# Optimization experiments

Measured on AMD Instinct MI355X. Metric: run time of the kernel, lower is better.

The kernel has to match this reference:

```python
import jax, jax.numpy as jnp
import numpy as np

N_NODES = 100000
N_EDGES = 1600000
IN_FEATS = 128
H1 = 256
H2 = 256
N_CLASSES = 64


def setup_inputs() -> dict:
    key = jax.random.key(0)
    ks = jax.random.split(key, 12)
    x = jax.random.normal(ks[0], (N_NODES, IN_FEATS), dtype=jnp.float32)
    src = jax.random.randint(ks[1], (N_EDGES,), 0, N_NODES, dtype=jnp.int64 if jax.config.jax_enable_x64 else jnp.int32)
    dst = jax.random.randint(ks[2], (N_EDGES,), 0, N_NODES, dtype=jnp.int64 if jax.config.jax_enable_x64 else jnp.int32)
    def lin(kw, kb, fan_in, fan_out):
        bound = 1.0 / np.sqrt(fan_in)
        W = jax.random.uniform(kw, (fan_out, fan_in), minval=-bound, maxval=bound, dtype=jnp.float32)
        b = jax.random.uniform(kb, (fan_out,), minval=-bound, maxval=bound, dtype=jnp.float32)
        return W, b
    W1, b1 = lin(ks[3], ks[4], 2 * IN_FEATS, H1)
    W2, b2 = lin(ks[5], ks[6], 2 * H1, H2)
    W3, b3 = lin(ks[7], ks[8], 2 * H2, N_CLASSES)
    return {"x": x, "src": src, "dst": dst,
            "W1": W1, "b1": b1, "W2": W2, "b2": b2, "W3": W3, "b3": b3}


def _sage_conv(h, src, dst, W, b):
    # message = copy from src node, reduce = mean at dst node (DGL copy_u + mean)
    m = jnp.take(h, src, axis=0)                                  # [E, d]
    s = jax.ops.segment_sum(m, dst, num_segments=N_NODES)         # [N, d]
    deg = jax.ops.segment_sum(jnp.ones((m.shape[0],), h.dtype), dst,
                              num_segments=N_NODES)               # [N]
    h_N = s / jnp.maximum(deg, 1.0)[:, None]                      # isolated nodes -> 0 (DGL behavior)
    h_total = jnp.concatenate([h, h_N], axis=1)                   # [N, 2d]
    return h_total @ W.T + b                                      # dropout inactive at eval (p=0.05)


def reference(x, src, dst, W1, b1, W2, b2, W3, b3):
    h = jax.nn.relu(_sage_conv(x, src, dst, W1, b1))
    h = jax.nn.relu(_sage_conv(h, src, dst, W2, b2))
    return _sage_conv(h, src, dst, W3, b3)
```

## Files before the change

kernel.cpp:

```cpp
#include <hip/hip_runtime.h>
#include <hip/hip_bf16.h>
#include <cstdint>
#include <cstddef>

#define N_NODES 100000
#define N_EDGES 1600000
#define NBUCK   128
#define NPB     782
#define NB_E    ((N_EDGES + 4095) / 4096)

#define FK_X    NB_E
#define FK_W1   (FK_X + 12500)
#define FK_W2   (FK_W1 + 64)
#define FK_W3   (FK_W2 + 128)
#define FK_END  (FK_W3 + 32)

typedef __attribute__((ext_vector_type(8))) short short8;
typedef __attribute__((ext_vector_type(4))) float floatx4;

__device__ inline float bf_lo(unsigned int u) { return __uint_as_float(u << 16); }
__device__ inline float bf_hi(unsigned int u) { return __uint_as_float(u & 0xffff0000u); }
__device__ inline unsigned short f2bf(float f) {
  unsigned int u = __float_as_uint(f);
  u += 0x7fffu + ((u >> 16) & 1u);
  return (unsigned short)(u >> 16);
}

__device__ inline void cvt4_body(const float* __restrict__ in,
                                 unsigned short* __restrict__ out, int t) {
  float4 v = ((const float4*)in)[t];
  ushort4 o;
  o.x = f2bf(v.x); o.y = f2bf(v.y); o.z = f2bf(v.z); o.w = f2bf(v.w);
  ((ushort4*)out)[t] = o;
}

__global__ __launch_bounds__(256)
void front_kernel(const int* __restrict__ dst, int* __restrict__ blockHist,
                  const float* __restrict__ x,  unsigned short* __restrict__ H0,
                  const float* __restrict__ W1, unsigned short* __restrict__ Wb1,
                  const float* __restrict__ W2, unsigned short* __restrict__ Wb2,
                  const float* __restrict__ W3, unsigned short* __restrict__ Wb3) {
  __shared__ int hist[NBUCK];
  const int b = blockIdx.x, tid = threadIdx.x;
  if (b < FK_X) {
    if (tid < NBUCK) hist[tid] = 0;
    __syncthreads();
#pragma unroll
    for (int i = 0; i < 16; ++i) {
      int e = b * 4096 + i * 256 + tid;
      if (e < N_EDGES) atomicAdd(&hist[dst[e] / NPB], 1);
    }
    __syncthreads();
    if (tid < NBUCK) blockHist[b * NBUCK + tid] = hist[tid];
  } else if (b < FK_W1) {
    cvt4_body(x, H0, (b - FK_X) * 256 + tid);
  } else if (b < FK_W2) {
    cvt4_body(W1, Wb1, (b - FK_W1) * 256 + tid);
  } else if (b < FK_W3) {
    cvt4_body(W2, Wb2, (b - FK_W2) * 256 + tid);
  } else {
    int t = (b - FK_W3) * 256 + tid;
    int idx4 = t * 4;
    int r = idx4 >> 8, c = idx4 & 255;
    float4 v = *(const float4*)(W3 + (size_t)(r & 63) * 512 + (r >> 6) * 256 + c);
    ushort4 o;
    o.x = f2bf(v.x); o.y = f2bf(v.y); o.z = f2bf(v.z); o.w = f2bf(v.w);
    *(ushort4*)(Wb3 + (size_t)r * 256 + c) = o;
  }
}

__device__ inline int wave_incl_scan(int v, int lane) {
#pragma unroll
  for (int off = 1; off < 64; off <<= 1) {
    int t = __shfl_up(v, off, 64);
    if (lane >= off) v += t;
  }
  return v;
}

__global__ void scanB_kernel(const int* __restrict__ blockHist,
                             int* __restrict__ bucketBase, int* __restrict__ blockOfs) {
  __shared__ int wsum[2];
  int t = threadIdx.x, lane = t & 63, wid = t >> 6;
  int total = 0;
#pragma unroll 4
  for (int blk = 0; blk < NB_E; ++blk) total += blockHist[blk * NBUCK + t];
  int incl = wave_incl_scan(total, lane);
  if (lane == 63) wsum[wid] = incl;
  __syncthreads();
  int off = (wid == 1) ? wsum[0] : 0;
  int base = off + incl - total;
  bucketBase[t] = base;
  if (t == 127) bucketBase[NBUCK] = off + incl;
  int running = base;
#pragma unroll 4
  for (int blk = 0; blk < NB_E; ++blk) {
    blockOfs[blk * NBUCK + t] = running;
    running += blockHist[blk * NBUCK + t];
  }
}

__global__ __launch_bounds__(256)
void pass1b_kernel(const int* __restrict__ src, const int* __restrict__ dst,
                   const int* __restrict__ blockOfs, unsigned int* __restrict__ staging) {
  __shared__ int hist[NBUCK];
  if (threadIdx.x < NBUCK) hist[threadIdx.x] = blockOfs[blockIdx.x * NBUCK + threadIdx.x];
  __syncthreads();
#pragma unroll
  for (int i = 0; i < 16; ++i) {
    int e = blockIdx.x * 4096 + i * 256 + threadIdx.x;
    if (e < N_EDGES) {
      int d = dst[e];
      int b = d / NPB;
      int pos = atomicAdd(&hist[b], 1);
      staging[pos] = (unsigned)src[e] | ((unsigned)(d - b * NPB) << 17);
    }
  }
}

__global__ __launch_bounds__(1024)
void pass2_kernel(const unsigned int* __restrict__ staging, const int* __restrict__ bucketBase,
                  int* __restrict__ start, float* __restrict__ invdeg,
                  int* __restrict__ esrc) {
  __shared__ int cnt[1024];
  __shared__ int cur[1024];
  __shared__ int wsum[16];
  const int b = blockIdx.x, tid = threadIdx.x;
  const int lane = tid & 63, wid = tid >> 6;
  const int n0 = b * NPB, n1 = min(n0 + NPB, N_NODES);
  const int nLocal = n1 - n0;
  const int p0 = bucketBase[b], p1 = bucketBase[b + 1];

  cnt[tid] = 0;
  __syncthreads();
  for (int e = p0 + tid; e < p1; e += 1024)
    atomicAdd(&cnt[staging[e] >> 17], 1);
  __syncthreads();

  int c = cnt[tid];
  int incl = wave_incl_scan(c, lane);
  if (lane == 63) wsum[wid] = incl;
  __syncthreads();
  if (wid == 0) {
    int v = (lane < 16) ? wsum[lane] : 0;
    int i2 = wave_incl_scan(v, lane);
    if (lane < 16) wsum[lane] = i2 - v;
  }
  __syncthreads();
  int excl = wsum[wid] + incl - c;
  cur[tid] = excl;
  if (tid < nLocal) {
    start[n0 + tid] = p0 + excl;
    invdeg[n0 + tid] = 1.0f / fmaxf((float)c, 1.0f);
  }
  if (b == NBUCK - 1 && tid == 0) start[N_NODES] = N_EDGES;
  __syncthreads();

  for (int e = p0 + tid; e < p1; e += 1024) {
    unsigned int pr = staging[e];
    int pos = p0 + atomicAdd(&cur[pr >> 17], 1);
    esrc[pos] = (int)(pr & 0x1FFFFu);
  }
}

template<int D>
__global__ __launch_bounds__(256)
void gather_mean(const unsigned short* __restrict__ h,
                 const int* __restrict__ start,
                 const int* __restrict__ esrc,
                 const float* __restrict__ invdeg,
                 unsigned short* __restrict__ hn) {
  int wave = (int)((blockIdx.x * 256 + threadIdx.x) >> 6);
  if (wave >= N_NODES) return;
  int lane = threadIdx.x & 63;
  int s0 = start[wave], s1 = start[wave + 1];
  constexpr int FPL = D / 64;
  float acc[FPL] = {};
  const unsigned short* base = h + lane * FPL;

  int e = s0;
  if constexpr (FPL == 4) {
    for (; e + 4 <= s1; e += 4) {
      int sn0 = esrc[e], sn1 = esrc[e + 1], sn2 = esrc[e + 2], sn3 = esrc[e + 3];
      uint2 p0 = *(const uint2*)(base + (size_t)sn0 * D);
      uint2 p1 = *(const uint2*)(base + (size_t)sn1 * D);
      uint2 p2 = *(const uint2*)(base + (size_t)sn2 * D);
      uint2 p3 = *(const uint2*)(base + (size_t)sn3 * D);
      acc[0] += bf_lo(p0.x) + bf_lo(p1.x) + bf_lo(p2.x) + bf_lo(p3.x);
      acc[1] += bf_hi(p0.x) + bf_hi(p1.x) + bf_hi(p2.x) + bf_hi(p3.x);
      acc[2] += bf_lo(p0.y) + bf_lo(p1.y) + bf_lo(p2.y) + bf_lo(p3.y);
      acc[3] += bf_hi(p0.y) + bf_hi(p1.y) + bf_hi(p2.y) + bf_hi(p3.y);
    }
    for (; e < s1; ++e) {
      int sn = esrc[e];
      uint2 p = *(const uint2*)(base + (size_t)sn * D);
      acc[0] += bf_lo(p.x); acc[1] += bf_hi(p.x);
      acc[2] += bf_lo(p.y); acc[3] += bf_hi(p.y);
    }
  } else {
    for (; e + 4 <= s1; e += 4) {
      int sn0 = esrc[e], sn1 = esrc[e + 1], sn2 = esrc[e + 2], sn3 = esrc[e + 3];
      unsigned int p0 = *(const unsigned int*)(base + (size_t)sn0 * D);
      unsigned int p1 = *(const unsigned int*)(base + (size_t)sn1 * D);
      unsigned int p2 = *(const unsigned int*)(base + (size_t)sn2 * D);
      unsigned int p3 = *(const unsigned int*)(base + (size_t)sn3 * D);
      acc[0] += bf_lo(p0) + bf_lo(p1) + bf_lo(p2) + bf_lo(p3);
      acc[1] += bf_hi(p0) + bf_hi(p1) + bf_hi(p2) + bf_hi(p3);
    }
    for (; e < s1; ++e) {
      int sn = esrc[e];
      unsigned int p = *(const unsigned int*)(base + (size_t)sn * D);
      acc[0] += bf_lo(p); acc[1] += bf_hi(p);
    }
  }

  float inv = invdeg[wave];
  unsigned short* out = hn + (size_t)wave * D + lane * FPL;
  if constexpr (FPL == 4) {
    ushort4 o;
    o.x = f2bf(acc[0] * inv); o.y = f2bf(acc[1] * inv);
    o.z = f2bf(acc[2] * inv); o.w = f2bf(acc[3] * inv);
    *(ushort4*)out = o;
  } else {
    ushort2 o;
    o.x = f2bf(acc[0] * inv); o.y = f2bf(acc[1] * inv);
    *(ushort2*)out = o;
  }
}

__global__ __launch_bounds__(256)
void gather_add64(const unsigned short* __restrict__ Y3,
                  const int* __restrict__ start, const int* __restrict__ esrc,
                  const float* __restrict__ invdeg, float* __restrict__ out) {
  int wave = (int)((blockIdx.x * 256 + threadIdx.x) >> 6);
  if (wave >= N_NODES) return;
  int lane = threadIdx.x & 63;
  int half = lane >> 5, l32 = lane & 31;
  int s0 = start[wave], s1 = start[wave + 1];
  const unsigned short* ybase = Y3 + 2 * l32;
  float a0 = 0.f, a1 = 0.f, b0 = 0.f, b1 = 0.f;
  for (int base = s0 + half; base < s1; base += 16) {
    unsigned int p[8];
#pragma unroll
    for (int k = 0; k < 8; ++k) {
      int e = base + 2 * k;
      p[k] = (e < s1) ? *(const unsigned int*)(ybase + (size_t)esrc[e] * 64) : 0u;
    }
#pragma unroll
    for (int k = 0; k < 8; k += 2) {
      a0 += bf_lo(p[k]);     a1 += bf_hi(p[k]);
      b0 += bf_lo(p[k + 1]); b1 += bf_hi(p[k + 1]);
    }
  }
  a0 += b0; a1 += b1;
  a0 += __shfl_xor(a0, 32, 64);
  a1 += __shfl_xor(a1, 32, 64);
  if (half == 0) {
    float inv = invdeg[wave];
    float2* q = (float2*)(out + (size_t)wave * 64 + 2 * l32);
    float2 v = *q;
    v.x += inv * a0; v.y += inv * a1;
    *q = v;
  }
}

template<int D, int DOUT, int BN, bool RELU, bool OUTF32, int MODE>
__global__ __launch_bounds__(256)
void sage_gemm(const unsigned short* __restrict__ H,
               const unsigned short* __restrict__ HN,
               const unsigned short* __restrict__ Wb,
               const float* __restrict__ bias,
               void* __restrict__ outp,
               unsigned short* __restrict__ y3) {
  constexpr int K   = (MODE == 1) ? D : 2 * D;
  constexpr int BM  = 128, KC = 32;
  constexpr int NCHUNK = K / KC;
  constexpr int AF  = BM / 16;
  constexpr int BF  = BN / 16;
  constexpr int FR  = AF + BF;
  constexpr int NMF = 4;
  constexpr int NJF = BF / 2;

  __shared__ __align__(16) unsigned short lds0[FR * 512];
  __shared__ __align__(16) unsigned short lds1[FR * 512];

  const int tid  = threadIdx.x;
  const int wave = tid >> 6, lane = tid & 63;
  const int l16  = lane & 15, quad = lane >> 4;
  const int n0   = blockIdx.x * BM;
  const int bn0  = blockIdx.y * BN;
  const int wm   = wave >> 1, wn = wave & 1;

  floatx4 acc[NMF][NJF] = {};

  auto stage = [&](int c, unsigned short* buf) {
    const int kc = c * KC;
    const unsigned short* srcH = (kc < D) ? H : HN;
    const int kb = (kc < D) ? kc : kc - D;
    const int w0 = __builtin_amdgcn_readfirstlane(wave);
#pragma unroll
    for (int i = 0; i < FR / 4; ++i) {
      const int fu = w0 + 4 * i;
      const unsigned short* g;
      if (fu < AF) {
        int row = min(n0 + fu * 16 + l16, N_NODES - 1);
        g = srcH + (size_t)row * D + kb + quad * 8;
      } else {
        int col = bn0 + (fu - AF) * 16 + l16;
        g = Wb + (size_t)col * K + kc + quad * 8;
      }
      __builtin_amdgcn_global_load_lds(
          (const __attribute__((address_space(1))) unsigned int*)g,
          (__attribute__((address_space(3))) unsigned int*)(buf + fu * 512),
          16, 0, 0);
    }
  };

  auto compute = [&](const unsigned short* buf) {
    short8 b[NJF];
#pragma unroll
    for (int jt = 0; jt < NJF; ++jt)
      b[jt] = *(const short8*)(buf + (AF + wn * NJF + jt) * 512 + lane * 8);
#pragma unroll
    for (int mi = 0; mi < NMF; ++mi) {
      short8 a = *(const short8*)(buf + (wm * NMF + mi) * 512 + lane * 8);
#pragma unroll
      for (int jt = 0; jt < NJF; ++jt)
        acc[mi][jt] = __builtin_amdgcn_mfma_f32_16x16x32_bf16(a, b[jt], acc[mi][jt], 0, 0, 0);
    }
  };

  stage(0, lds0);
  __syncthreads();
#pragma unroll 1
  for (int c = 0; c < NCHUNK; c += 2) {
    stage(c + 1, lds1);
    compute(lds0);
    __syncthreads();
    if (c + 2 < NCHUNK) stage(c + 2, lds0);
    compute(lds1);
    __syncthreads();
  }

#pragma unroll
  for (int mi = 0; mi < NMF; ++mi) {
#pragma unroll
    for (int jt = 0; jt < NJF; ++jt) {
      int j = bn0 + wn * (NJF * 16) + jt * 16 + l16;
      float bj = (MODE == 1 && wn == 1) ? 0.0f : bias[j];
#pragma unroll
      for (int r = 0; r < 4; ++r) {
        int node = n0 + wm * 64 + mi * 16 + quad * 4 + r;
        if (node < N_NODES) {
          float v = acc[mi][jt][r];
          if constexpr (MODE == 1) {
            if (wn == 0) ((float*)outp)[(size_t)node * 64 + j] = v + bj;
            else y3[(size_t)node * 64 + (j - 64)] = f2bf(v);
          } else {
            v += bj;
            if (RELU) v = fmaxf(v, 0.0f);
            if (OUTF32) ((float*)outp)[(size_t)node * DOUT + j] = v;
            else ((unsigned short*)outp)[(size_t)node * DOUT + j] = f2bf(v);
          }
        }
      }
    }
  }
}

extern "C" void kernel_launch(void* const* d_in, const int* in_sizes, int n_in,
                              void* d_out, int out_size, void* d_ws, size_t ws_size,
                              hipStream_t stream) {
  const float* x   = (const float*)d_in[0];
  const int*   src = (const int*)d_in[1];
  const int*   dst = (const int*)d_in[2];
  const float* W1 = (const float*)d_in[3];
  const float* b1 = (const float*)d_in[4];
  const float* W2 = (const float*)d_in[5];
  const float* b2 = (const float*)d_in[6];
  const float* W3 = (const float*)d_in[7];
  const float* b3 = (const float*)d_in[8];

  char* ws = (char*)d_ws;
  unsigned short* H0 = (unsigned short*)ws; ws += (size_t)N_NODES * 128 * 2;
  unsigned short* H1 = (unsigned short*)ws; ws += (size_t)N_NODES * 256 * 2;
  unsigned short* H2 = (unsigned short*)ws; ws += (size_t)N_NODES * 256 * 2;
  unsigned short* HN = (unsigned short*)ws; ws += (size_t)N_NODES * 256 * 2;
  unsigned int* staging = (unsigned int*)ws; ws += (size_t)N_EDGES * 4;
  int* esrc   = (int*)ws;  ws += (size_t)N_EDGES * 4;
  int* startp = (int*)ws;  ws += (size_t)(N_NODES + 32) * 4;
  float* invdeg = (float*)ws; ws += (size_t)(N_NODES + 32) * 4;
  int* bucketBase  = (int*)ws; ws += 1024;
  int* blockHist   = (int*)ws; ws += (size_t)NB_E * NBUCK * 4;
  int* blockOfs    = (int*)ws; ws += (size_t)NB_E * NBUCK * 4;
  unsigned short* Y3 = (unsigned short*)ws; ws += (size_t)N_NODES * 64 * 2;
  unsigned short* Wb1 = (unsigned short*)ws; ws += 256 * 256 * 2;
  unsigned short* Wb2 = (unsigned short*)ws; ws += 256 * 512 * 2;
  unsigned short* Wb3 = (unsigned short*)ws; ws += 128 * 256 * 2;

  front_kernel<<<FK_END, 256, 0, stream>>>(dst, blockHist, x, H0, W1, Wb1, W2, Wb2, W3, Wb3);
  scanB_kernel<<<1, 128, 0, stream>>>(blockHist, bucketBase, blockOfs);
  pass1b_kernel<<<NB_E, 256, 0, stream>>>(src, dst, blockOfs, staging);
  pass2_kernel<<<NBUCK, 1024, 0, stream>>>(staging, bucketBase, startp, invdeg, esrc);

  const int GGRID = (N_NODES * 64 + 255) / 256;
  const int MG = (N_NODES + 127) / 128;

  gather_mean<128><<<GGRID, 256, 0, stream>>>(H0, startp, esrc, invdeg, HN);
  sage_gemm<128, 256, 128, true, false, 0><<<dim3(MG, 2), 256, 0, stream>>>(H0, HN, Wb1, b1, H1, nullptr);

  gather_mean<256><<<GGRID, 256, 0, stream>>>(H1, startp, esrc, invdeg, HN);
  sage_gemm<256, 256, 128, true, false, 0><<<dim3(MG, 2), 256, 0, stream>>>(H1, HN, Wb2, b2, H2, nullptr);

  sage_gemm<256, 128, 128, false, true, 1><<<dim3(MG, 1), 256, 0, stream>>>(H2, nullptr, Wb3, b3, (float*)d_out, Y3);
  gather_add64<<<GGRID, 256, 0, stream>>>(Y3, startp, esrc, invdeg, (float*)d_out);
}
```

Baseline: 613.8 us.

## Parallelize bucket offset scan across waves and simplify final gather loop

The single-block serial scan over edge-block histograms is split into a wave-per-bucket parallel scan that writes local block offsets and bucket counts. A tiny second kernel then scans the bucket counts, and pass1b adds the bucket base when it loads the offsets. The final 64-wide gather loop is also restructured into a 4-way unrolled loop with a scalar tail, replacing the predicated 8-load batch. This adds one kernel launch, and the gather now keeps fewer loads in flight per iteration.

```diff
diff --git a/kernel.cpp b/kernel.cpp
--- a/kernel.cpp
+++ b/kernel.cpp
@@ -78,33 +78,43 @@
   return v;
 }
 
-__global__ void scanB_kernel(const int* __restrict__ blockHist,
-                             int* __restrict__ bucketBase, int* __restrict__ blockOfs) {
+__global__ __launch_bounds__(256)
+void scanB1_kernel(const int* __restrict__ blockHist,
+                   int* __restrict__ blockOfs, int* __restrict__ bucketCount) {
+  int bucket = (int)((blockIdx.x * 256 + threadIdx.x) >> 6);
+  if (bucket >= NBUCK) return;
+  int lane = threadIdx.x & 63;
+  int carry = 0;
+  for (int c0 = 0; c0 < NB_E; c0 += 64) {
+    int blk = c0 + lane;
+    int v = (blk < NB_E) ? blockHist[blk * NBUCK + bucket] : 0;
+    int incl = wave_incl_scan(v, lane);
+    if (blk < NB_E) blockOfs[blk * NBUCK + bucket] = carry + incl - v;
+    carry += __shfl(incl, 63, 64);
+  }
+  if (lane == 63) bucketCount[bucket] = carry;
+}
+
+__global__ void scanB2_kernel(const int* __restrict__ bucketCount,
+                              int* __restrict__ bucketBase) {
   __shared__ int wsum[2];
   int t = threadIdx.x, lane = t & 63, wid = t >> 6;
-  int total = 0;
-#pragma unroll 4
-  for (int blk = 0; blk < NB_E; ++blk) total += blockHist[blk * NBUCK + t];
-  int incl = wave_incl_scan(total, lane);
+  int v = bucketCount[t];
+  int incl = wave_incl_scan(v, lane);
   if (lane == 63) wsum[wid] = incl;
   __syncthreads();
   int off = (wid == 1) ? wsum[0] : 0;
-  int base = off + incl - total;
-  bucketBase[t] = base;
+  bucketBase[t] = off + incl - v;
   if (t == 127) bucketBase[NBUCK] = off + incl;
-  int running = base;
-#pragma unroll 4
-  for (int blk = 0; blk < NB_E; ++blk) {
-    blockOfs[blk * NBUCK + t] = running;
-    running += blockHist[blk * NBUCK + t];
-  }
 }
 
 __global__ __launch_bounds__(256)
 void pass1b_kernel(const int* __restrict__ src, const int* __restrict__ dst,
-                   const int* __restrict__ blockOfs, unsigned int* __restrict__ staging) {
+                   const int* __restrict__ blockOfs, const int* __restrict__ bucketBase,
+                   unsigned int* __restrict__ staging) {
   __shared__ int hist[NBUCK];
-  if (threadIdx.x < NBUCK) hist[threadIdx.x] = blockOfs[blockIdx.x * NBUCK + threadIdx.x];
+  if (threadIdx.x < NBUCK)
+    hist[threadIdx.x] = bucketBase[threadIdx.x] + blockOfs[blockIdx.x * NBUCK + threadIdx.x];
   __syncthreads();
 #pragma unroll
   for (int i = 0; i < 16; ++i) {
@@ -239,18 +249,23 @@
   int s0 = start[wave], s1 = start[wave + 1];
   const unsigned short* ybase = Y3 + 2 * l32;
   float a0 = 0.f, a1 = 0.f, b0 = 0.f, b1 = 0.f;
-  for (int base = s0 + half; base < s1; base += 16) {
-    unsigned int p[8];
-#pragma unroll
-    for (int k = 0; k < 8; ++k) {
-      int e = base + 2 * k;
-      p[k] = (e < s1) ? *(const unsigned int*)(ybase + (size_t)esrc[e] * 64) : 0u;
-    }
-#pragma unroll
-    for (int k = 0; k < 8; k += 2) {
-      a0 += bf_lo(p[k]);     a1 += bf_hi(p[k]);
-      b0 += bf_lo(p[k + 1]); b1 += bf_hi(p[k + 1]);
-    }
+  int e = s0 + half;
+  for (; e + 6 < s1; e += 8) {
+    int sn0 = esrc[e],     sn1 = esrc[e + 2];
+    int sn2 = esrc[e + 4], sn3 = esrc[e + 6];
+    unsigned int p0 = *(const unsigned int*)(ybase + (size_t)sn0 * 64);
+    unsigned int p1 = *(const unsigned int*)(ybase + (size_t)sn1 * 64);
+    unsigned int p2 = *(const unsigned int*)(ybase + (size_t)sn2 * 64);
+    unsigned int p3 = *(const unsigned int*)(ybase + (size_t)sn3 * 64);
+    a0 += bf_lo(p0) + bf_lo(p2);
+    a1 += bf_hi(p0) + bf_hi(p2);
+    b0 += bf_lo(p1) + bf_lo(p3);
+    b1 += bf_hi(p1) + bf_hi(p3);
+  }
+  for (; e < s1; e += 2) {
+    int sn = esrc[e];
+    unsigned int p = *(const unsigned int*)(ybase + (size_t)sn * 64);
+    a0 += bf_lo(p); a1 += bf_hi(p);
   }
   a0 += b0; a1 += b1;
   a0 += __shfl_xor(a0, 32, 64);
@@ -391,6 +406,7 @@
   int* startp = (int*)ws;  ws += (size_t)(N_NODES + 32) * 4;
   float* invdeg = (float*)ws; ws += (size_t)(N_NODES + 32) * 4;
   int* bucketBase  = (int*)ws; ws += 1024;
+  int* bucketCount = (int*)ws; ws += 512;
   int* blockHist   = (int*)ws; ws += (size_t)NB_E * NBUCK * 4;
   int* blockOfs    = (int*)ws; ws += (size_t)NB_E * NBUCK * 4;
   unsigned short* Y3 = (unsigned short*)ws; ws += (size_t)N_NODES * 64 * 2;
@@ -399,8 +415,9 @@
   unsigned short* Wb3 = (unsigned short*)ws; ws += 128 * 256 * 2;
 
   front_kernel<<<FK_END, 256, 0, stream>>>(dst, blockHist, x, H0, W1, Wb1, W2, Wb2, W3, Wb3);
-  scanB_kernel<<<1, 128, 0, stream>>>(blockHist, bucketBase, blockOfs);
-  pass1b_kernel<<<NB_E, 256, 0, stream>>>(src, dst, blockOfs, staging);
+  scanB1_kernel<<<(NBUCK * 64 + 255) / 256, 256, 0, stream>>>(blockHist, blockOfs, bucketCount);
+  scanB2_kernel<<<1, 128, 0, stream>>>(bucketCount, bucketBase);
+  pass1b_kernel<<<NB_E, 256, 0, stream>>>(src, dst, blockOfs, bucketBase, staging);
   pass2_kernel<<<NBUCK, 1024, 0, stream>>>(staging, bucketBase, startp, invdeg, esrc);
 
   const int GGRID = (N_NODES * 64 + 255) / 256;
```

Measured after the change: 557.7 us. 9.1% less time.
